# Optimization experiments

Measured on AMD Instinct MI355X. Metric: run time of the kernel, lower is better.

Reference implementation:

```python
import jax, jax.numpy as jnp
import numpy as np

N_NODES = 10000


def _gcn_norm(edge_index, n):
    # PyG GCNConv default: add self-loops, symmetric deg^{-1/2} normalization
    src, dst = edge_index[0], edge_index[1]
    loop = jnp.arange(n, dtype=edge_index.dtype)
    src = jnp.concatenate([src, loop])
    dst = jnp.concatenate([dst, loop])
    deg = jax.ops.segment_sum(jnp.ones_like(dst, dtype=jnp.float32), dst, num_segments=n)
    inv_sqrt = jnp.where(deg > 0, jax.lax.rsqrt(jnp.maximum(deg, 1e-12)), 0.0)
    norm = inv_sqrt[src] * inv_sqrt[dst]  # [E + N]
    return src, dst, norm


def _gcn_conv(x, W, b, src, dst, norm, n):
    h = x @ W                              # [N, out]
    msg = h[src] * norm[:, None]           # gather + scale  [E+N, out]
    out = jax.ops.segment_sum(msg, dst, num_segments=n)  # scatter-add
    return out + b


def setup_inputs() -> dict:
    key = jax.random.key(0)
    ks = jax.random.split(key, 8)
    n, e = N_NODES, 640000
    cin, ch, cout = 128, 128, 64

    def glorot(k, fan_in, fan_out):
        s = float(np.sqrt(6.0 / (fan_in + fan_out)))
        return jax.random.uniform(k, (fan_in, fan_out), jnp.float32, -s, s)

    return {
        "x": jax.random.normal(ks[0], (n, cin), jnp.float32),
        "edge_index": jax.random.randint(ks[1], (2, e), 0, n, jnp.int64),
        "W1": glorot(ks[2], cin, ch),
        "b1": jnp.zeros((ch,), jnp.float32),
        "W2": glorot(ks[3], ch, ch),
        "b2": jnp.zeros((ch,), jnp.float32),
        "W3": glorot(ks[4], ch, cout),
        "b3": jnp.zeros((cout,), jnp.float32),
    }


def reference(x, edge_index, W1, b1, W2, b2, W3, b3):
    n = x.shape[0]
    src, dst, norm = _gcn_norm(edge_index, n)
    h = jax.nn.relu(_gcn_conv(x, W1, b1, src, dst, norm, n))
    h = jax.nn.relu(_gcn_conv(h, W2, b2, src, dst, norm, n))
    return _gcn_conv(h, W3, b3, src, dst, norm, n)
```

## Files before the change

### kernel.cpp

```cpp
#include <hip/hip_runtime.h>

#define NN 10000
#define NE 640000
#define NB 313
#define RSTRIDE 2688
#define EPB 2048
#define G1B 1250

__device__ __forceinline__ unsigned short f2bf(float x) {
    unsigned u = __float_as_uint(x);
    u += 0x7FFFu + ((u >> 16) & 1u);
    return (unsigned short)(u >> 16);
}
__device__ __forceinline__ float bflo(unsigned u) { return __uint_as_float(u << 16); }
__device__ __forceinline__ float bfhi(unsigned u) { return __uint_as_float(u & 0xFFFF0000u); }
__device__ __forceinline__ float bf1(unsigned short h) { return __uint_as_float((unsigned)h << 16); }

struct SMpart { int hist[NB]; int scanv[NB + 1]; int gbase[NB]; int lcur[NB];
                unsigned stage[EPB]; };
struct SMbuild { int sbase[NB + 1]; int hist32[32]; int cur32[32];
                 unsigned stage[RSTRIDE]; };
union SMu {
    SMpart p;
    SMbuild b;
    float xs[16][128];
    float2 red2[3][64];
    float red1[3][64];
};

__device__ __forceinline__ void gemm1_block(const float* __restrict__ X,
                                            const float* __restrict__ W,
                                            unsigned short* __restrict__ Y,
                                            float (*xs)[128], int vb, int tid) {
    int row0 = vb * 8;
    for (int idx = tid; idx < 8 * 128; idx += 256) {
        int r = idx >> 7, k = idx & 127;
        xs[r][k] = X[(size_t)(row0 + r) * 128 + k];
    }
    __syncthreads();
    int ct = tid & 31, r = tid >> 5, c = ct * 4;
    float4 acc = make_float4(0.f, 0.f, 0.f, 0.f);
    #pragma unroll 8
    for (int k = 0; k < 128; ++k) {
        float xv = xs[r][k];
        float4 w = *reinterpret_cast<const float4*>(W + (size_t)k * 128 + c);
        acc.x += xv * w.x; acc.y += xv * w.y; acc.z += xv * w.z; acc.w += xv * w.w;
    }
    ushort4 o;
    o.x = f2bf(acc.x); o.y = f2bf(acc.y); o.z = f2bf(acc.z); o.w = f2bf(acc.w);
    *reinterpret_cast<ushort4*>(Y + (size_t)(row0 + r) * 128 + c) = o;
}

template<int NOUTc, int ROWS>
__device__ __forceinline__ void gemm_bf_block(const unsigned short* __restrict__ Xb,
                                              const float* __restrict__ W,
                                              unsigned short* __restrict__ Y,
                                              float (*xs)[128], int vb, int tid) {
    int row0 = vb * ROWS;
    const unsigned* Xu = reinterpret_cast<const unsigned*>(Xb + (size_t)row0 * 128);
    for (int idx = tid; idx < ROWS * 64; idx += 256) {
        unsigned u = Xu[idx];
        int r = idx >> 6, kk = idx & 63;
        xs[r][kk * 2]     = bflo(u);
        xs[r][kk * 2 + 1] = bfhi(u);
    }
    __syncthreads();
    constexpr int COLT = NOUTc / 4;
    int ct = tid % COLT, r = tid / COLT, c = ct * 4;
    float4 acc = make_float4(0.f, 0.f, 0.f, 0.f);
    #pragma unroll 8
    for (int k = 0; k < 128; ++k) {
        float xv = xs[r][k];
        float4 w = *reinterpret_cast<const float4*>(W + (size_t)k * NOUTc + c);
        acc.x += xv * w.x; acc.y += xv * w.y; acc.z += xv * w.z; acc.w += xv * w.w;
    }
    ushort4 o;
    o.x = f2bf(acc.x); o.y = f2bf(acc.y); o.z = f2bf(acc.z); o.w = f2bf(acc.w);
    *reinterpret_cast<ushort4*>(Y + (size_t)(row0 + r) * NOUTc + c) = o;
}

__device__ __forceinline__ void partition_block(const int* __restrict__ src,
                                                const int* __restrict__ dst,
                                                int* __restrict__ bcur,
                                                unsigned* __restrict__ edge_part,
                                                SMpart& p, int bid, int tid) {
    for (int i = tid; i < NB; i += 256) p.hist[i] = 0;
    __syncthreads();
    int gi = bid * EPB + tid * 8;
    unsigned rec[8];
    bool act = gi < NE;
    if (act) {
        int4 s0 = *reinterpret_cast<const int4*>(src + gi);
        int4 s1 = *reinterpret_cast<const int4*>(src + gi + 4);
        int4 d0 = *reinterpret_cast<const int4*>(dst + gi);
        int4 d1 = *reinterpret_cast<const int4*>(dst + gi + 4);
        rec[0] = ((unsigned)d0.x << 14) | (unsigned)s0.x;
        rec[1] = ((unsigned)d0.y << 14) | (unsigned)s0.y;
        rec[2] = ((unsigned)d0.z << 14) | (unsigned)s0.z;
        rec[3] = ((unsigned)d0.w << 14) | (unsigned)s0.w;
        rec[4] = ((unsigned)d1.x << 14) | (unsigned)s1.x;
        rec[5] = ((unsigned)d1.y << 14) | (unsigned)s1.y;
        rec[6] = ((unsigned)d1.z << 14) | (unsigned)s1.z;
        rec[7] = ((unsigned)d1.w << 14) | (unsigned)s1.w;
        #pragma unroll
        for (int k = 0; k < 8; ++k) atomicAdd(&p.hist[rec[k] >> 19], 1);
    }
    __syncthreads();
    if (tid < 64) {
        int carry = 0;
        for (int c = 0; c < NB; c += 64) {
            int idx = c + tid;
            int v = (idx < NB) ? p.hist[idx] : 0;
            int incl = v;
            #pragma unroll
            for (int d = 1; d < 64; d <<= 1) {
                int t = __shfl_up(incl, d, 64);
                if (tid >= d) incl += t;
            }
            if (idx < NB) p.scanv[idx] = carry + incl - v;
            carry += __shfl(incl, 63, 64);
        }
        if (tid == 0) p.scanv[NB] = carry;
    }
    __syncthreads();
    for (int bb = tid; bb < NB; bb += 256) {
        p.gbase[bb] = atomicAdd(&bcur[bb], p.hist[bb]);
        p.lcur[bb]  = p.scanv[bb];
    }
    __syncthreads();
    if (act) {
        #pragma unroll
        for (int k = 0; k < 8; ++k) {
            int bb = rec[k] >> 19;
            int pp = atomicAdd(&p.lcur[bb], 1);
            p.stage[pp] = rec[k];
        }
    }
    __syncthreads();
    int tot = p.scanv[NB];
    for (int i = tid; i < tot; i += 256) {
        unsigned r = p.stage[i];
        int bb = r >> 19;
        edge_part[bb * RSTRIDE + p.gbase[bb] + (i - p.scanv[bb])] = r;
    }
}

__device__ __forceinline__ void build_block(const unsigned* __restrict__ edge_part,
                                            const int* __restrict__ bcur,
                                            int* __restrict__ offs,
                                            float* __restrict__ inv_sqrt,
                                            unsigned short* __restrict__ edge_src,
                                            SMbuild& b, int bid, int tid) {
    if (tid < 64) {
        int carry = 0;
        for (int c = 0; c < NB; c += 64) {
            int idx = c + tid;
            int v = (idx < NB) ? bcur[idx] : 0;
            int incl = v;
            #pragma unroll
            for (int d = 1; d < 64; d <<= 1) {
                int t = __shfl_up(incl, d, 64);
                if (tid >= d) incl += t;
            }
            if (idx < NB) b.sbase[idx] = carry + incl - v;
            carry += __shfl(incl, 63, 64);
        }
    }
    if (tid < 32) b.hist32[tid] = 0;
    __syncthreads();
    int cnt = bcur[bid];
    int base = b.sbase[bid];
    const unsigned* part = edge_part + (size_t)bid * RSTRIDE;
    for (int k = tid; k < cnt; k += 256)
        atomicAdd(&b.hist32[(part[k] >> 14) & 31], 1);
    __syncthreads();
    if (tid < 32) {
        int v = b.hist32[tid];
        int incl = v;
        #pragma unroll
        for (int d = 1; d < 32; d <<= 1) {
            int t = __shfl_up(incl, d, 32);
            if (tid >= d) incl += t;
        }
        int excl = incl - v;
        b.cur32[tid] = excl;
        int node = bid * 32 + tid;
        if (node < NN) {
            offs[node] = base + excl;
            inv_sqrt[node] = rsqrtf((float)(v + 1));
        }
        if (bid == NB - 1 && tid == 0) offs[NN] = base + cnt;
    }
    __syncthreads();
    for (int k = tid; k < cnt; k += 256) {
        unsigned r = part[k];
        int pp = atomicAdd(&b.cur32[(r >> 14) & 31], 1);
        b.stage[pp] = r & 0x3FFFu;
    }
    __syncthreads();
    for (int k = tid; k < cnt; k += 256)
        edge_src[base + k] = (unsigned short)b.stage[k];
}

__device__ __forceinline__ void agg128_node(const unsigned short* __restrict__ H,
                                            unsigned* __restrict__ Aout,
                                            float bx, float by,
                                            const int* __restrict__ offs,
                                            const float* __restrict__ isqv,
                                            const unsigned short* __restrict__ esrc,
                                            float2 (*red)[64], int node,
                                            int lane, int wv) {
    int s = offs[node], e = offs[node + 1];
    int deg = e - s;
    int qlen = (((deg + 3) >> 2) + 3) & ~3;
    int js = s + wv * qlen;
    int je = js + qlen;
    if (js > e) js = e;
    if (je > e) je = e;
    int col = lane * 2;
    float2 acc = make_float2(0.f, 0.f);
    int j = js;
    for (; j + 4 <= je; j += 4) {
        int s0 = esrc[j], s1 = esrc[j + 1], s2 = esrc[j + 2], s3 = esrc[j + 3];
        float w0 = isqv[s0], w1 = isqv[s1], w2 = isqv[s2], w3 = isqv[s3];
        unsigned u0 = *reinterpret_cast<const unsigned*>(H + (size_t)s0 * 128 + col);
        unsigned u1 = *reinterpret_cast<const unsigned*>(H + (size_t)s1 * 128 + col);
        unsigned u2 = *reinterpret_cast<const unsigned*>(H + (size_t)s2 * 128 + col);
        unsigned u3 = *reinterpret_cast<const unsigned*>(H + (size_t)s3 * 128 + col);
        acc.x += w0 * bflo(u0); acc.y += w0 * bfhi(u0);
        acc.x += w1 * bflo(u1); acc.y += w1 * bfhi(u1);
        acc.x += w2 * bflo(u2); acc.y += w2 * bfhi(u2);
        acc.x += w3 * bflo(u3); acc.y += w3 * bfhi(u3);
    }
    for (; j < je; ++j) {
        int s0 = esrc[j];
        float w0 = isqv[s0];
        unsigned u0 = *reinterpret_cast<const unsigned*>(H + (size_t)s0 * 128 + col);
        acc.x += w0 * bflo(u0); acc.y += w0 * bfhi(u0);
    }
    if (wv) red[wv - 1][lane] = acc;
    __syncthreads();
    if (!wv) {
        acc.x += red[0][lane].x + red[1][lane].x + red[2][lane].x;
        acc.y += red[0][lane].y + red[1][lane].y + red[2][lane].y;
        float isq = isqv[node];
        unsigned uv = *reinterpret_cast<const unsigned*>(H + (size_t)node * 128 + col);
        float self = isq * isq;
        float ox = fmaxf(acc.x * isq + self * bflo(uv) + bx, 0.f);
        float oy = fmaxf(acc.y * isq + self * bfhi(uv) + by, 0.f);
        Aout[(size_t)node * 64 + lane] = (unsigned)f2bf(ox) | ((unsigned)f2bf(oy) << 16);
    }
}

__device__ __forceinline__ void agg64_node(const unsigned short* __restrict__ H,
                                           float* __restrict__ out, float b3v,
                                           const int* __restrict__ offs,
                                           const float* __restrict__ isqv,
                                           const unsigned short* __restrict__ esrc,
                                           float (*red)[64], int node,
                                           int lane, int wv) {
    int s = offs[node], e = offs[node + 1];
    int deg = e - s;
    int qlen = (((deg + 3) >> 2) + 3) & ~3;
    int js = s + wv * qlen;
    int je = js + qlen;
    if (js > e) js = e;
    if (je > e) je = e;
    float acc = 0.f;
    int j = js;
    for (; j + 4 <= je; j += 4) {
        int s0 = esrc[j], s1 = esrc[j + 1], s2 = esrc[j + 2], s3 = esrc[j + 3];
        float w0 = isqv[s0], w1 = isqv[s1], w2 = isqv[s2], w3 = isqv[s3];
        acc += w0 * bf1(H[(size_t)s0 * 64 + lane]);
        acc += w1 * bf1(H[(size_t)s1 * 64 + lane]);
        acc += w2 * bf1(H[(size_t)s2 * 64 + lane]);
        acc += w3 * bf1(H[(size_t)s3 * 64 + lane]);
    }
    for (; j < je; ++j) {
        int s0 = esrc[j];
        acc += isqv[s0] * bf1(H[(size_t)s0 * 64 + lane]);
    }
    if (wv) red[wv - 1][lane] = acc;
    __syncthreads();
    if (!wv) {
        acc += red[0][lane] + red[1][lane] + red[2][lane];
        float isq = isqv[node];
        float hv = bf1(H[(size_t)node * 64 + lane]);
        out[(size_t)node * 64 + lane] = acc * isq + isq * isq * hv + b3v;
    }
}

__global__ __launch_bounds__(256) void part_gemm1_kernel(
        const int* __restrict__ src, const int* __restrict__ dst,
        int* __restrict__ bcur, unsigned* __restrict__ edge_part,
        const float* __restrict__ X, const float* __restrict__ W,
        unsigned short* __restrict__ Y) {
    __shared__ SMu sm;
    int tid = threadIdx.x;
    if (blockIdx.x >= NB) {
        gemm1_block(X, W, Y, sm.xs, blockIdx.x - NB, tid);
        return;
    }
    partition_block(src, dst, bcur, edge_part, sm.p, blockIdx.x, tid);
}

__global__ __launch_bounds__(256) void build_kernel(
        const unsigned* __restrict__ edge_part, const int* __restrict__ bcur,
        int* __restrict__ offs, float* __restrict__ inv_sqrt,
        unsigned short* __restrict__ edge_src) {
    __shared__ SMu sm;
    build_block(edge_part, bcur, offs, inv_sqrt, edge_src, sm.b,
                blockIdx.x, threadIdx.x);
}

__global__ __launch_bounds__(256) void agg128_kernel(
        const unsigned short* __restrict__ H, const unsigned short* __restrict__ esrc,
        const int* __restrict__ offs, const float* __restrict__ inv_sqrt,
        const float* __restrict__ bias, unsigned* __restrict__ Aout) {
    __shared__ SMu sm;
    int tid = threadIdx.x, lane = tid & 63, wv = tid >> 6;
    int col = lane * 2;
    agg128_node(H, Aout, bias[col], bias[col + 1], offs, inv_sqrt, esrc,
                sm.red2, blockIdx.x, lane, wv);
}

__global__ __launch_bounds__(256) void agg64_kernel(
        const unsigned short* __restrict__ H, const unsigned short* __restrict__ esrc,
        const int* __restrict__ offs, const float* __restrict__ inv_sqrt,
        const float* __restrict__ bias, float* __restrict__ out) {
    __shared__ SMu sm;
    int tid = threadIdx.x, lane = tid & 63, wv = tid >> 6;
    agg64_node(H, out, bias[lane], offs, inv_sqrt, esrc,
               sm.red1, blockIdx.x, lane, wv);
}

template<int N>
__global__ __launch_bounds__(256) void gemm_bf_kernel(
        const unsigned short* __restrict__ X, const float* __restrict__ W,
        unsigned short* __restrict__ Y) {
    __shared__ SMu sm;
    gemm_bf_block<N, 256 / (N / 4)>(X, W, Y, sm.xs, blockIdx.x, threadIdx.x);
}

extern "C" void kernel_launch(void* const* d_in, const int* in_sizes, int n_in,
                              void* d_out, int out_size, void* d_ws, size_t ws_size,
                              hipStream_t stream) {
    const float* x  = (const float*)d_in[0];
    const int*   ei = (const int*)d_in[1];
    const float* W1 = (const float*)d_in[2];
    const float* b1 = (const float*)d_in[3];
    const float* W2 = (const float*)d_in[4];
    const float* b2 = (const float*)d_in[5];
    const float* W3 = (const float*)d_in[6];
    const float* b3 = (const float*)d_in[7];
    float* out = (float*)d_out;

    const int* src = ei;
    const int* dst = ei + NE;

    char* ws = (char*)d_ws;
    int*            bcur      = (int*)(ws);
    float*          inv_sqrt  = (float*)(ws + 4096);
    int*            offs      = (int*)(ws + 45056);
    unsigned*       edge_part = (unsigned*)(ws + 86016);
    unsigned short* edge_src  = (unsigned short*)(ws + 3451392);
    unsigned short* T1        = (unsigned short*)(ws + 6011392);
    unsigned short* A         = (unsigned short*)(ws + 8571392);
    unsigned short* T2        = (unsigned short*)edge_part;
    unsigned short* T3        = T1;

    hipMemsetAsync(bcur, 0, NB * sizeof(int), stream);
    part_gemm1_kernel<<<NB + G1B, 256, 0, stream>>>(src, dst, bcur, edge_part,
                                                    x, W1, T1);
    build_kernel<<<NB, 256, 0, stream>>>(edge_part, bcur, offs, inv_sqrt, edge_src);
    agg128_kernel<<<NN, 256, 0, stream>>>(T1, edge_src, offs, inv_sqrt, b1,
                                          (unsigned*)A);
    gemm_bf_kernel<128><<<NN / 8, 256, 0, stream>>>(A, W2, T2);
    agg128_kernel<<<NN, 256, 0, stream>>>(T2, edge_src, offs, inv_sqrt, b2,
                                          (unsigned*)A);
    gemm_bf_kernel<64><<<NN / 16, 256, 0, stream>>>(A, W3, T3);
    agg64_kernel<<<NN, 256, 0, stream>>>(T3, edge_src, offs, inv_sqrt, b3, out);
}
```

Baseline: 149.0 us.

## Fuse aggregation with following GEMM and rebalance waves per node

Each aggregation over 128 channels is merged with the next layer's weight multiply. A 1024-thread block handles 8 nodes with two waves per node, stages the ReLU'd rows in shared memory, then multiplies them by W. This drops the intermediate A buffer round trip and two kernel launches. The final 64-channel aggregation now uses 128-thread blocks with two waves per node, and the memset is replaced by a tiny zeroing kernel. The trade-off is that fewer waves split the edge loop of each node, and the large blocks may limit occupancy or leave threads idle during the GEMM phase.

```diff
diff --git a/kernel.cpp b/kernel.cpp
--- a/kernel.cpp
+++ b/kernel.cpp
@@ -23,10 +23,12 @@
 union SMu {
     SMpart p;
     SMbuild b;
-    float xs[16][128];
-    float2 red2[3][64];
-    float red1[3][64];
+    float xs[8][128];
 };
+
+__global__ void zero_kernel(int* __restrict__ cur) {
+    if (threadIdx.x < NB) cur[threadIdx.x] = 0;
+}
 
 __device__ __forceinline__ void gemm1_block(const float* __restrict__ X,
                                             const float* __restrict__ W,
@@ -49,34 +51,6 @@
     ushort4 o;
     o.x = f2bf(acc.x); o.y = f2bf(acc.y); o.z = f2bf(acc.z); o.w = f2bf(acc.w);
     *reinterpret_cast<ushort4*>(Y + (size_t)(row0 + r) * 128 + c) = o;
-}
-
-template<int NOUTc, int ROWS>
-__device__ __forceinline__ void gemm_bf_block(const unsigned short* __restrict__ Xb,
-                                              const float* __restrict__ W,
-                                              unsigned short* __restrict__ Y,
-                                              float (*xs)[128], int vb, int tid) {
-    int row0 = vb * ROWS;
-    const unsigned* Xu = reinterpret_cast<const unsigned*>(Xb + (size_t)row0 * 128);
-    for (int idx = tid; idx < ROWS * 64; idx += 256) {
-        unsigned u = Xu[idx];
-        int r = idx >> 6, kk = idx & 63;
-        xs[r][kk * 2]     = bflo(u);
-        xs[r][kk * 2 + 1] = bfhi(u);
-    }
-    __syncthreads();
-    constexpr int COLT = NOUTc / 4;
-    int ct = tid % COLT, r = tid / COLT, c = ct * 4;
-    float4 acc = make_float4(0.f, 0.f, 0.f, 0.f);
-    #pragma unroll 8
-    for (int k = 0; k < 128; ++k) {
-        float xv = xs[r][k];
-        float4 w = *reinterpret_cast<const float4*>(W + (size_t)k * NOUTc + c);
-        acc.x += xv * w.x; acc.y += xv * w.y; acc.z += xv * w.z; acc.w += xv * w.w;
-    }
-    ushort4 o;
-    o.x = f2bf(acc.x); o.y = f2bf(acc.y); o.z = f2bf(acc.z); o.w = f2bf(acc.w);
-    *reinterpret_cast<ushort4*>(Y + (size_t)(row0 + r) * NOUTc + c) = o;
 }
 
 __device__ __forceinline__ void partition_block(const int* __restrict__ src,
@@ -202,21 +176,49 @@
         edge_src[base + k] = (unsigned short)b.stage[k];
 }
 
-__device__ __forceinline__ void agg128_node(const unsigned short* __restrict__ H,
-                                            unsigned* __restrict__ Aout,
-                                            float bx, float by,
-                                            const int* __restrict__ offs,
-                                            const float* __restrict__ isqv,
-                                            const unsigned short* __restrict__ esrc,
-                                            float2 (*red)[64], int node,
-                                            int lane, int wv) {
+__global__ __launch_bounds__(256) void part_gemm1_kernel(
+        const int* __restrict__ src, const int* __restrict__ dst,
+        int* __restrict__ bcur, unsigned* __restrict__ edge_part,
+        const float* __restrict__ X, const float* __restrict__ W,
+        unsigned short* __restrict__ Y) {
+    __shared__ SMu sm;
+    int tid = threadIdx.x;
+    if (blockIdx.x >= NB) {
+        gemm1_block(X, W, Y, sm.xs, blockIdx.x - NB, tid);
+        return;
+    }
+    partition_block(src, dst, bcur, edge_part, sm.p, blockIdx.x, tid);
+}
+
+__global__ __launch_bounds__(256) void build_kernel(
+        const unsigned* __restrict__ edge_part, const int* __restrict__ bcur,
+        int* __restrict__ offs, float* __restrict__ inv_sqrt,
+        unsigned short* __restrict__ edge_src) {
+    __shared__ SMu sm;
+    build_block(edge_part, bcur, offs, inv_sqrt, edge_src, sm.b,
+                blockIdx.x, threadIdx.x);
+}
+
+template<int NOUTc>
+__global__ __launch_bounds__(1024) void agg_gemm_kernel(
+        const unsigned short* __restrict__ H,
+        const unsigned short* __restrict__ esrc,
+        const int* __restrict__ offs, const float* __restrict__ isqv,
+        const float* __restrict__ bias, const float* __restrict__ W,
+        unsigned* __restrict__ Yu) {
+    __shared__ float As[8][128];
+    __shared__ float2 red[8][64];
+    int tid = threadIdx.x;
+    int lane = tid & 63;
+    int w = tid >> 6;
+    int nl = w >> 1, sub = w & 1;
+    int node = blockIdx.x * 8 + nl;
     int s = offs[node], e = offs[node + 1];
     int deg = e - s;
-    int qlen = (((deg + 3) >> 2) + 3) & ~3;
-    int js = s + wv * qlen;
-    int je = js + qlen;
-    if (js > e) js = e;
-    if (je > e) je = e;
+    int half = ((deg >> 1) + 3) & ~3;
+    int js = s + sub * half;
+    int mid = s + half;
+    int je = sub ? e : (mid < e ? mid : e);
     int col = lane * 2;
     float2 acc = make_float2(0.f, 0.f);
     int j = js;
@@ -238,39 +240,53 @@
         unsigned u0 = *reinterpret_cast<const unsigned*>(H + (size_t)s0 * 128 + col);
         acc.x += w0 * bflo(u0); acc.y += w0 * bfhi(u0);
     }
-    if (wv) red[wv - 1][lane] = acc;
-    __syncthreads();
-    if (!wv) {
-        acc.x += red[0][lane].x + red[1][lane].x + red[2][lane].x;
-        acc.y += red[0][lane].y + red[1][lane].y + red[2][lane].y;
+    if (sub) red[nl][lane] = acc;
+    __syncthreads();
+    if (!sub) {
+        acc.x += red[nl][lane].x;
+        acc.y += red[nl][lane].y;
         float isq = isqv[node];
         unsigned uv = *reinterpret_cast<const unsigned*>(H + (size_t)node * 128 + col);
         float self = isq * isq;
-        float ox = fmaxf(acc.x * isq + self * bflo(uv) + bx, 0.f);
-        float oy = fmaxf(acc.y * isq + self * bfhi(uv) + by, 0.f);
-        Aout[(size_t)node * 64 + lane] = (unsigned)f2bf(ox) | ((unsigned)f2bf(oy) << 16);
-    }
-}
-
-__device__ __forceinline__ void agg64_node(const unsigned short* __restrict__ H,
-                                           float* __restrict__ out, float b3v,
-                                           const int* __restrict__ offs,
-                                           const float* __restrict__ isqv,
-                                           const unsigned short* __restrict__ esrc,
-                                           float (*red)[64], int node,
-                                           int lane, int wv) {
+        As[nl][col]     = fmaxf(acc.x * isq + self * bflo(uv) + bias[col], 0.f);
+        As[nl][col + 1] = fmaxf(acc.y * isq + self * bfhi(uv) + bias[col + 1], 0.f);
+    }
+    __syncthreads();
+    constexpr int PC = NOUTc / 2;
+    if (tid < 8 * PC) {
+        int r = tid / PC, pc = tid % PC, c = pc * 2;
+        float2 a2 = make_float2(0.f, 0.f);
+        #pragma unroll 8
+        for (int k = 0; k < 128; ++k) {
+            float xv = As[r][k];
+            float2 wv2 = *reinterpret_cast<const float2*>(W + (size_t)k * NOUTc + c);
+            a2.x += xv * wv2.x;
+            a2.y += xv * wv2.y;
+        }
+        int gr = blockIdx.x * 8 + r;
+        Yu[(size_t)gr * PC + pc] = (unsigned)f2bf(a2.x) | ((unsigned)f2bf(a2.y) << 16);
+    }
+}
+
+__global__ __launch_bounds__(128) void agg64_kernel(
+        const unsigned short* __restrict__ H, const unsigned short* __restrict__ esrc,
+        const int* __restrict__ offs, const float* __restrict__ inv_sqrt,
+        const float* __restrict__ bias, float* __restrict__ out) {
+    __shared__ float red[64];
+    int node = blockIdx.x;
+    int tid = threadIdx.x, lane = tid & 63, wv = tid >> 6;
     int s = offs[node], e = offs[node + 1];
     int deg = e - s;
-    int qlen = (((deg + 3) >> 2) + 3) & ~3;
-    int js = s + wv * qlen;
-    int je = js + qlen;
-    if (js > e) js = e;
-    if (je > e) je = e;
+    int half = ((deg >> 1) + 3) & ~3;
+    int js = s + wv * half;
+    int mid = s + half;
+    int je = wv ? e : (mid < e ? mid : e);
     float acc = 0.f;
     int j = js;
     for (; j + 4 <= je; j += 4) {
         int s0 = esrc[j], s1 = esrc[j + 1], s2 = esrc[j + 2], s3 = esrc[j + 3];
-        float w0 = isqv[s0], w1 = isqv[s1], w2 = isqv[s2], w3 = isqv[s3];
+        float w0 = inv_sqrt[s0], w1 = inv_sqrt[s1];
+        float w2 = inv_sqrt[s2], w3 = inv_sqrt[s3];
         acc += w0 * bf1(H[(size_t)s0 * 64 + lane]);
         acc += w1 * bf1(H[(size_t)s1 * 64 + lane]);
         acc += w2 * bf1(H[(size_t)s2 * 64 + lane]);
@@ -278,68 +294,16 @@
     }
     for (; j < je; ++j) {
         int s0 = esrc[j];
-        acc += isqv[s0] * bf1(H[(size_t)s0 * 64 + lane]);
-    }
-    if (wv) red[wv - 1][lane] = acc;
+        acc += inv_sqrt[s0] * bf1(H[(size_t)s0 * 64 + lane]);
+    }
+    if (wv) red[lane] = acc;
     __syncthreads();
     if (!wv) {
-        acc += red[0][lane] + red[1][lane] + red[2][lane];
-        float isq = isqv[node];
+        acc += red[lane];
+        float isq = inv_sqrt[node];
         float hv = bf1(H[(size_t)node * 64 + lane]);
-        out[(size_t)node * 64 + lane] = acc * isq + isq * isq * hv + b3v;
-    }
-}
-
-__global__ __launch_bounds__(256) void part_gemm1_kernel(
-        const int* __restrict__ src, const int* __restrict__ dst,
-        int* __restrict__ bcur, unsigned* __restrict__ edge_part,
-        const float* __restrict__ X, const float* __restrict__ W,
-        unsigned short* __restrict__ Y) {
-    __shared__ SMu sm;
-    int tid = threadIdx.x;
-    if (blockIdx.x >= NB) {
-        gemm1_block(X, W, Y, sm.xs, blockIdx.x - NB, tid);
-        return;
-    }
-    partition_block(src, dst, bcur, edge_part, sm.p, blockIdx.x, tid);
-}
-
-__global__ __launch_bounds__(256) void build_kernel(
-        const unsigned* __restrict__ edge_part, const int* __restrict__ bcur,
-        int* __restrict__ offs, float* __restrict__ inv_sqrt,
-        unsigned short* __restrict__ edge_src) {
-    __shared__ SMu sm;
-    build_block(edge_part, bcur, offs, inv_sqrt, edge_src, sm.b,
-                blockIdx.x, threadIdx.x);
-}
-
-__global__ __launch_bounds__(256) void agg128_kernel(
-        const unsigned short* __restrict__ H, const unsigned short* __restrict__ esrc,
-        const int* __restrict__ offs, const float* __restrict__ inv_sqrt,
-        const float* __restrict__ bias, unsigned* __restrict__ Aout) {
-    __shared__ SMu sm;
-    int tid = threadIdx.x, lane = tid & 63, wv = tid >> 6;
-    int col = lane * 2;
-    agg128_node(H, Aout, bias[col], bias[col + 1], offs, inv_sqrt, esrc,
-                sm.red2, blockIdx.x, lane, wv);
-}
-
-__global__ __launch_bounds__(256) void agg64_kernel(
-        const unsigned short* __restrict__ H, const unsigned short* __restrict__ esrc,
-        const int* __restrict__ offs, const float* __restrict__ inv_sqrt,
-        const float* __restrict__ bias, float* __restrict__ out) {
-    __shared__ SMu sm;
-    int tid = threadIdx.x, lane = tid & 63, wv = tid >> 6;
-    agg64_node(H, out, bias[lane], offs, inv_sqrt, esrc,
-               sm.red1, blockIdx.x, lane, wv);
-}
-
-template<int N>
-__global__ __launch_bounds__(256) void gemm_bf_kernel(
-        const unsigned short* __restrict__ X, const float* __restrict__ W,
-        unsigned short* __restrict__ Y) {
-    __shared__ SMu sm;
-    gemm_bf_block<N, 256 / (N / 4)>(X, W, Y, sm.xs, blockIdx.x, threadIdx.x);
+        out[(size_t)node * 64 + lane] = acc * isq + isq * isq * hv + bias[lane];
+    }
 }
 
 extern "C" void kernel_launch(void* const* d_in, const int* in_sizes, int n_in,
@@ -365,19 +329,16 @@
     unsigned*       edge_part = (unsigned*)(ws + 86016);
     unsigned short* edge_src  = (unsigned short*)(ws + 3451392);
     unsigned short* T1        = (unsigned short*)(ws + 6011392);
-    unsigned short* A         = (unsigned short*)(ws + 8571392);
     unsigned short* T2        = (unsigned short*)edge_part;
     unsigned short* T3        = T1;
 
-    hipMemsetAsync(bcur, 0, NB * sizeof(int), stream);
+    zero_kernel<<<1, 320, 0, stream>>>(bcur);
     part_gemm1_kernel<<<NB + G1B, 256, 0, stream>>>(src, dst, bcur, edge_part,
                                                     x, W1, T1);
     build_kernel<<<NB, 256, 0, stream>>>(edge_part, bcur, offs, inv_sqrt, edge_src);
-    agg128_kernel<<<NN, 256, 0, stream>>>(T1, edge_src, offs, inv_sqrt, b1,
-                                          (unsigned*)A);
-    gemm_bf_kernel<128><<<NN / 8, 256, 0, stream>>>(A, W2, T2);
-    agg128_kernel<<<NN, 256, 0, stream>>>(T2, edge_src, offs, inv_sqrt, b2,
-                                          (unsigned*)A);
-    gemm_bf_kernel<64><<<NN / 16, 256, 0, stream>>>(A, W3, T3);
-    agg64_kernel<<<NN, 256, 0, stream>>>(T3, edge_src, offs, inv_sqrt, b3, out);
-}
+    agg_gemm_kernel<128><<<NN / 8, 1024, 0, stream>>>(T1, edge_src, offs, inv_sqrt,
+                                                      b1, W2, (unsigned*)T2);
+    agg_gemm_kernel<64><<<NN / 8, 1024, 0, stream>>>(T2, edge_src, offs, inv_sqrt,
+                                                     b2, W3, (unsigned*)T3);
+    agg64_kernel<<<NN, 128, 0, stream>>>(T3, edge_src, offs, inv_sqrt, b3, out);
+}
```

Result: slower. 165.8 us (+11.3%).

## Rework aggregation kernels to 2 waves with half-wave edge split and wider loads

Applied to the files above, without the earlier changes.

The aggregation kernels now use 128-thread blocks (two waves) instead of four waves. Each wave splits into two half-waves that handle alternating edges, with wider per-lane loads (8 bytes of bf16 for the 128-wide features). Partial sums are combined with a cross-half shuffle plus one small shared-memory exchange, and the memset is replaced by a tiny zeroing kernel. The goal is to cut the reduction and synchronisation overhead per node and issue fewer, wider gather loads, at the cost of fewer waves per node to hide gather latency.

```diff
diff --git a/kernel.cpp b/kernel.cpp
--- a/kernel.cpp
+++ b/kernel.cpp
@@ -14,7 +14,6 @@
 }
 __device__ __forceinline__ float bflo(unsigned u) { return __uint_as_float(u << 16); }
 __device__ __forceinline__ float bfhi(unsigned u) { return __uint_as_float(u & 0xFFFF0000u); }
-__device__ __forceinline__ float bf1(unsigned short h) { return __uint_as_float((unsigned)h << 16); }
 
 struct SMpart { int hist[NB]; int scanv[NB + 1]; int gbase[NB]; int lcur[NB];
                 unsigned stage[EPB]; };
@@ -24,9 +23,11 @@
     SMpart p;
     SMbuild b;
     float xs[16][128];
-    float2 red2[3][64];
-    float red1[3][64];
 };
+
+__global__ void zero_kernel(int* __restrict__ cur) {
+    if (threadIdx.x < NB) cur[threadIdx.x] = 0;
+}
 
 __device__ __forceinline__ void gemm1_block(const float* __restrict__ X,
                                             const float* __restrict__ W,
@@ -202,94 +203,6 @@
         edge_src[base + k] = (unsigned short)b.stage[k];
 }
 
-__device__ __forceinline__ void agg128_node(const unsigned short* __restrict__ H,
-                                            unsigned* __restrict__ Aout,
-                                            float bx, float by,
-                                            const int* __restrict__ offs,
-                                            const float* __restrict__ isqv,
-                                            const unsigned short* __restrict__ esrc,
-                                            float2 (*red)[64], int node,
-                                            int lane, int wv) {
-    int s = offs[node], e = offs[node + 1];
-    int deg = e - s;
-    int qlen = (((deg + 3) >> 2) + 3) & ~3;
-    int js = s + wv * qlen;
-    int je = js + qlen;
-    if (js > e) js = e;
-    if (je > e) je = e;
-    int col = lane * 2;
-    float2 acc = make_float2(0.f, 0.f);
-    int j = js;
-    for (; j + 4 <= je; j += 4) {
-        int s0 = esrc[j], s1 = esrc[j + 1], s2 = esrc[j + 2], s3 = esrc[j + 3];
-        float w0 = isqv[s0], w1 = isqv[s1], w2 = isqv[s2], w3 = isqv[s3];
-        unsigned u0 = *reinterpret_cast<const unsigned*>(H + (size_t)s0 * 128 + col);
-        unsigned u1 = *reinterpret_cast<const unsigned*>(H + (size_t)s1 * 128 + col);
-        unsigned u2 = *reinterpret_cast<const unsigned*>(H + (size_t)s2 * 128 + col);
-        unsigned u3 = *reinterpret_cast<const unsigned*>(H + (size_t)s3 * 128 + col);
-        acc.x += w0 * bflo(u0); acc.y += w0 * bfhi(u0);
-        acc.x += w1 * bflo(u1); acc.y += w1 * bfhi(u1);
-        acc.x += w2 * bflo(u2); acc.y += w2 * bfhi(u2);
-        acc.x += w3 * bflo(u3); acc.y += w3 * bfhi(u3);
-    }
-    for (; j < je; ++j) {
-        int s0 = esrc[j];
-        float w0 = isqv[s0];
-        unsigned u0 = *reinterpret_cast<const unsigned*>(H + (size_t)s0 * 128 + col);
-        acc.x += w0 * bflo(u0); acc.y += w0 * bfhi(u0);
-    }
-    if (wv) red[wv - 1][lane] = acc;
-    __syncthreads();
-    if (!wv) {
-        acc.x += red[0][lane].x + red[1][lane].x + red[2][lane].x;
-        acc.y += red[0][lane].y + red[1][lane].y + red[2][lane].y;
-        float isq = isqv[node];
-        unsigned uv = *reinterpret_cast<const unsigned*>(H + (size_t)node * 128 + col);
-        float self = isq * isq;
-        float ox = fmaxf(acc.x * isq + self * bflo(uv) + bx, 0.f);
-        float oy = fmaxf(acc.y * isq + self * bfhi(uv) + by, 0.f);
-        Aout[(size_t)node * 64 + lane] = (unsigned)f2bf(ox) | ((unsigned)f2bf(oy) << 16);
-    }
-}
-
-__device__ __forceinline__ void agg64_node(const unsigned short* __restrict__ H,
-                                           float* __restrict__ out, float b3v,
-                                           const int* __restrict__ offs,
-                                           const float* __restrict__ isqv,
-                                           const unsigned short* __restrict__ esrc,
-                                           float (*red)[64], int node,
-                                           int lane, int wv) {
-    int s = offs[node], e = offs[node + 1];
-    int deg = e - s;
-    int qlen = (((deg + 3) >> 2) + 3) & ~3;
-    int js = s + wv * qlen;
-    int je = js + qlen;
-    if (js > e) js = e;
-    if (je > e) je = e;
-    float acc = 0.f;
-    int j = js;
-    for (; j + 4 <= je; j += 4) {
-        int s0 = esrc[j], s1 = esrc[j + 1], s2 = esrc[j + 2], s3 = esrc[j + 3];
-        float w0 = isqv[s0], w1 = isqv[s1], w2 = isqv[s2], w3 = isqv[s3];
-        acc += w0 * bf1(H[(size_t)s0 * 64 + lane]);
-        acc += w1 * bf1(H[(size_t)s1 * 64 + lane]);
-        acc += w2 * bf1(H[(size_t)s2 * 64 + lane]);
-        acc += w3 * bf1(H[(size_t)s3 * 64 + lane]);
-    }
-    for (; j < je; ++j) {
-        int s0 = esrc[j];
-        acc += isqv[s0] * bf1(H[(size_t)s0 * 64 + lane]);
-    }
-    if (wv) red[wv - 1][lane] = acc;
-    __syncthreads();
-    if (!wv) {
-        acc += red[0][lane] + red[1][lane] + red[2][lane];
-        float isq = isqv[node];
-        float hv = bf1(H[(size_t)node * 64 + lane]);
-        out[(size_t)node * 64 + lane] = acc * isq + isq * isq * hv + b3v;
-    }
-}
-
 __global__ __launch_bounds__(256) void part_gemm1_kernel(
         const int* __restrict__ src, const int* __restrict__ dst,
         int* __restrict__ bcur, unsigned* __restrict__ edge_part,
@@ -313,25 +226,136 @@
                 blockIdx.x, threadIdx.x);
 }
 
-__global__ __launch_bounds__(256) void agg128_kernel(
+__global__ __launch_bounds__(128) void agg128_kernel(
         const unsigned short* __restrict__ H, const unsigned short* __restrict__ esrc,
-        const int* __restrict__ offs, const float* __restrict__ inv_sqrt,
+        const int* __restrict__ offs, const float* __restrict__ isqv,
         const float* __restrict__ bias, unsigned* __restrict__ Aout) {
-    __shared__ SMu sm;
+    __shared__ float4 red[32];
+    int node = blockIdx.x;
     int tid = threadIdx.x, lane = tid & 63, wv = tid >> 6;
-    int col = lane * 2;
-    agg128_node(H, Aout, bias[col], bias[col + 1], offs, inv_sqrt, esrc,
-                sm.red2, blockIdx.x, lane, wv);
-}
-
-__global__ __launch_bounds__(256) void agg64_kernel(
+    int l = lane & 31, g = lane >> 5;
+    int s = offs[node], e = offs[node + 1];
+    int deg = e - s;
+    int half = ((deg >> 1) + 7) & ~7;
+    int js = s + wv * half;
+    if (js > e) js = e;
+    int mid = s + half;
+    int je = wv ? e : (mid < e ? mid : e);
+    int colb = l * 4;
+    float4 acc = make_float4(0.f, 0.f, 0.f, 0.f);
+    int j = js;
+    for (; j + 8 <= je; j += 8) {
+        int sA = esrc[j + g],     sB = esrc[j + 2 + g];
+        int sC = esrc[j + 4 + g], sD = esrc[j + 6 + g];
+        float wA = isqv[sA], wB = isqv[sB], wC = isqv[sC], wD = isqv[sD];
+        uint2 a = *reinterpret_cast<const uint2*>(H + (size_t)sA * 128 + colb);
+        uint2 b = *reinterpret_cast<const uint2*>(H + (size_t)sB * 128 + colb);
+        uint2 c = *reinterpret_cast<const uint2*>(H + (size_t)sC * 128 + colb);
+        uint2 d = *reinterpret_cast<const uint2*>(H + (size_t)sD * 128 + colb);
+        acc.x += wA * bflo(a.x); acc.y += wA * bfhi(a.x);
+        acc.z += wA * bflo(a.y); acc.w += wA * bfhi(a.y);
+        acc.x += wB * bflo(b.x); acc.y += wB * bfhi(b.x);
+        acc.z += wB * bflo(b.y); acc.w += wB * bfhi(b.y);
+        acc.x += wC * bflo(c.x); acc.y += wC * bfhi(c.x);
+        acc.z += wC * bflo(c.y); acc.w += wC * bfhi(c.y);
+        acc.x += wD * bflo(d.x); acc.y += wD * bfhi(d.x);
+        acc.z += wD * bflo(d.y); acc.w += wD * bfhi(d.y);
+    }
+    for (; j + 2 <= je; j += 2) {
+        int sA = esrc[j + g];
+        float wA = isqv[sA];
+        uint2 a = *reinterpret_cast<const uint2*>(H + (size_t)sA * 128 + colb);
+        acc.x += wA * bflo(a.x); acc.y += wA * bfhi(a.x);
+        acc.z += wA * bflo(a.y); acc.w += wA * bfhi(a.y);
+    }
+    if (j < je && g == 0) {
+        int sA = esrc[j];
+        float wA = isqv[sA];
+        uint2 a = *reinterpret_cast<const uint2*>(H + (size_t)sA * 128 + colb);
+        acc.x += wA * bflo(a.x); acc.y += wA * bfhi(a.x);
+        acc.z += wA * bflo(a.y); acc.w += wA * bfhi(a.y);
+    }
+    acc.x += __shfl_down(acc.x, 32);
+    acc.y += __shfl_down(acc.y, 32);
+    acc.z += __shfl_down(acc.z, 32);
+    acc.w += __shfl_down(acc.w, 32);
+    if (wv == 1 && lane < 32) red[lane] = acc;
+    __syncthreads();
+    if (wv == 0 && lane < 32) {
+        float4 r = red[lane];
+        acc.x += r.x; acc.y += r.y; acc.z += r.z; acc.w += r.w;
+        float isq = isqv[node];
+        uint2 uv = *reinterpret_cast<const uint2*>(H + (size_t)node * 128 + colb);
+        float self = isq * isq;
+        float o0 = fmaxf(acc.x * isq + self * bflo(uv.x) + bias[colb],     0.f);
+        float o1 = fmaxf(acc.y * isq + self * bfhi(uv.x) + bias[colb + 1], 0.f);
+        float o2 = fmaxf(acc.z * isq + self * bflo(uv.y) + bias[colb + 2], 0.f);
+        float o3 = fmaxf(acc.w * isq + self * bfhi(uv.y) + bias[colb + 3], 0.f);
+        uint2 ov;
+        ov.x = (unsigned)f2bf(o0) | ((unsigned)f2bf(o1) << 16);
+        ov.y = (unsigned)f2bf(o2) | ((unsigned)f2bf(o3) << 16);
+        *reinterpret_cast<uint2*>(Aout + (size_t)node * 64 + l * 2) = ov;
+    }
+}
+
+__global__ __launch_bounds__(128) void agg64_kernel(
         const unsigned short* __restrict__ H, const unsigned short* __restrict__ esrc,
-        const int* __restrict__ offs, const float* __restrict__ inv_sqrt,
+        const int* __restrict__ offs, const float* __restrict__ isqv,
         const float* __restrict__ bias, float* __restrict__ out) {
-    __shared__ SMu sm;
+    __shared__ float2 red[32];
+    int node = blockIdx.x;
     int tid = threadIdx.x, lane = tid & 63, wv = tid >> 6;
-    agg64_node(H, out, bias[lane], offs, inv_sqrt, esrc,
-               sm.red1, blockIdx.x, lane, wv);
+    int l = lane & 31, g = lane >> 5;
+    int s = offs[node], e = offs[node + 1];
+    int deg = e - s;
+    int half = ((deg >> 1) + 7) & ~7;
+    int js = s + wv * half;
+    if (js > e) js = e;
+    int mid = s + half;
+    int je = wv ? e : (mid < e ? mid : e);
+    int colb = l * 2;
+    float2 acc = make_float2(0.f, 0.f);
+    int j = js;
+    for (; j + 8 <= je; j += 8) {
+        int sA = esrc[j + g],     sB = esrc[j + 2 + g];
+        int sC = esrc[j + 4 + g], sD = esrc[j + 6 + g];
+        float wA = isqv[sA], wB = isqv[sB], wC = isqv[sC], wD = isqv[sD];
+        unsigned a = *reinterpret_cast<const unsigned*>(H + (size_t)sA * 64 + colb);
+        unsigned b = *reinterpret_cast<const unsigned*>(H + (size_t)sB * 64 + colb);
+        unsigned c = *reinterpret_cast<const unsigned*>(H + (size_t)sC * 64 + colb);
+        unsigned d = *reinterpret_cast<const unsigned*>(H + (size_t)sD * 64 + colb);
+        acc.x += wA * bflo(a); acc.y += wA * bfhi(a);
+        acc.x += wB * bflo(b); acc.y += wB * bfhi(b);
+        acc.x += wC * bflo(c); acc.y += wC * bfhi(c);
+        acc.x += wD * bflo(d); acc.y += wD * bfhi(d);
+    }
+    for (; j + 2 <= je; j += 2) {
+        int sA = esrc[j + g];
+        float wA = isqv[sA];
+        unsigned a = *reinterpret_cast<const unsigned*>(H + (size_t)sA * 64 + colb);
+        acc.x += wA * bflo(a); acc.y += wA * bfhi(a);
+    }
+    if (j < je && g == 0) {
+        int sA = esrc[j];
+        float wA = isqv[sA];
+        unsigned a = *reinterpret_cast<const unsigned*>(H + (size_t)sA * 64 + colb);
+        acc.x += wA * bflo(a); acc.y += wA * bfhi(a);
+    }
+    acc.x += __shfl_down(acc.x, 32);
+    acc.y += __shfl_down(acc.y, 32);
+    if (wv == 1 && lane < 32) red[lane] = acc;
+    __syncthreads();
+    if (wv == 0 && lane < 32) {
+        float2 r = red[lane];
+        acc.x += r.x; acc.y += r.y;
+        float isq = isqv[node];
+        unsigned uv = *reinterpret_cast<const unsigned*>(H + (size_t)node * 64 + colb);
+        float self = isq * isq;
+        float2 ov;
+        ov.x = acc.x * isq + self * bflo(uv) + bias[colb];
+        ov.y = acc.y * isq + self * bfhi(uv) + bias[colb + 1];
+        *reinterpret_cast<float2*>(out + (size_t)node * 64 + colb) = ov;
+    }
 }
 
 template<int N>
@@ -369,15 +393,15 @@
     unsigned short* T2        = (unsigned short*)edge_part;
     unsigned short* T3        = T1;
 
-    hipMemsetAsync(bcur, 0, NB * sizeof(int), stream);
+    zero_kernel<<<1, 320, 0, stream>>>(bcur);
     part_gemm1_kernel<<<NB + G1B, 256, 0, stream>>>(src, dst, bcur, edge_part,
                                                     x, W1, T1);
     build_kernel<<<NB, 256, 0, stream>>>(edge_part, bcur, offs, inv_sqrt, edge_src);
-    agg128_kernel<<<NN, 256, 0, stream>>>(T1, edge_src, offs, inv_sqrt, b1,
+    agg128_kernel<<<NN, 128, 0, stream>>>(T1, edge_src, offs, inv_sqrt, b1,
                                           (unsigned*)A);
     gemm_bf_kernel<128><<<NN / 8, 256, 0, stream>>>(A, W2, T2);
-    agg128_kernel<<<NN, 256, 0, stream>>>(T2, edge_src, offs, inv_sqrt, b2,
+    agg128_kernel<<<NN, 128, 0, stream>>>(T2, edge_src, offs, inv_sqrt, b2,
                                           (unsigned*)A);
     gemm_bf_kernel<64><<<NN / 16, 256, 0, stream>>>(A, W3, T3);
-    agg64_kernel<<<NN, 256, 0, stream>>>(T3, edge_src, offs, inv_sqrt, b3, out);
-}
+    agg64_kernel<<<NN, 128, 0, stream>>>(T3, edge_src, offs, inv_sqrt, b3, out);
+}
```

New measurement: 133.2 us. 1.12x faster.
